# Optimization experiments

Measured on AMD Instinct MI355X. Metric: run time of the kernel, lower is better.

## Reference

```python
import jax, jax.numpy as jnp
import numpy as np

B, H, W, DIM = 8, 32, 32, 768
HEADS = 12
HD = DIM // HEADS  # 64


def setup_inputs() -> dict:
    key = jax.random.key(0)
    ks = jax.random.split(key, 7)
    s = 0.02  # init scale to keep logits in a sane range
    return {
        "x": jax.random.normal(ks[0], (B, H, W, DIM), jnp.float32),
        "qkv_w": jax.random.normal(ks[1], (3 * DIM, DIM), jnp.float32) * s,
        "qkv_b": jax.random.normal(ks[2], (3 * DIM,), jnp.float32) * s,
        "proj_w": jax.random.normal(ks[3], (DIM, DIM), jnp.float32) * s,
        "proj_b": jax.random.normal(ks[4], (DIM,), jnp.float32) * s,
        "rel_pos_h": jax.random.normal(ks[5], (2 * H - 1, HD), jnp.float32) * s,
        "rel_pos_w": jax.random.normal(ks[6], (2 * W - 1, HD), jnp.float32) * s,
    }


def reference(x, qkv_w, qkv_b, proj_w, proj_b, rel_pos_h, rel_pos_w):
    b, h, w, dim = x.shape
    n = h * w
    hd = dim // HEADS
    scale = hd ** -0.5

    xf = x.reshape(b, n, dim)
    qkv = xf @ qkv_w.T + qkv_b                       # (B, N, 3*dim)
    qkv = qkv.reshape(b, n, 3, HEADS, hd)
    qkv = jnp.transpose(qkv, (2, 0, 3, 1, 4)).reshape(3, b * HEADS, n, hd)
    q, k, v = qkv[0], qkv[1], qkv[2]                 # each (B*heads, N, hd)

    # decomposed rel-pos bias (q_size == k_size -> pure index lookup)
    coords_h = jnp.arange(h)[:, None] - jnp.arange(h)[None, :] + (h - 1)
    coords_w = jnp.arange(w)[:, None] - jnp.arange(w)[None, :] + (w - 1)
    Rh = rel_pos_h[coords_h]                         # (H, H, hd)
    Rw = rel_pos_w[coords_w]                         # (W, W, hd)
    r_q = q.reshape(b * HEADS, h, w, hd)
    rel_h = jnp.einsum('bhwc,hkc->bhwk', r_q, Rh)    # (B*heads, H, W, H)
    rel_w = jnp.einsum('bhwc,wkc->bhwk', r_q, Rw)    # (B*heads, H, W, W)
    bias = (rel_h[:, :, :, :, None] + rel_w[:, :, :, None, :]).reshape(b * HEADS, n, n)

    attn = (q * scale) @ jnp.swapaxes(k, -2, -1) + bias
    attn = jax.nn.softmax(attn, axis=-1)
    out = attn @ v                                   # (B*heads, N, hd)

    out = out.reshape(b, HEADS, n, hd)
    out = jnp.transpose(out, (0, 2, 1, 3)).reshape(b, n, dim)
    out = out @ proj_w.T + proj_b
    return out.reshape(b, h, w, dim)
```

## Files before the change

### kernel.cpp

```cpp
#include <hip/hip_runtime.h>
#include <hip/hip_bf16.h>

typedef unsigned short u16;
typedef __attribute__((ext_vector_type(8))) short bf16x8;
typedef __attribute__((ext_vector_type(4))) short s16x4;
typedef __attribute__((ext_vector_type(4))) float f32x4;

#define QSCALE 0.18033688011116012f
#define RPSCALE 8.0f
#define EXP2(x) __builtin_amdgcn_exp2f(x)

__device__ __forceinline__ float bf2f(u16 u) {
  union { unsigned int i; float f; } v; v.i = ((unsigned int)u) << 16; return v.f;
}
__device__ __forceinline__ u16 f2bf(float f) {
  union { float f; unsigned int i; } v; v.f = f;
  unsigned int r = v.i + 0x7fffu + ((v.i >> 16) & 1u);
  return (u16)(r >> 16);
}
__device__ __forceinline__ unsigned int pk2bf(float a, float b) {
  union { __hip_bfloat162 h; unsigned int u; } cv;
  cv.h = __float22bfloat162_rn(float2{a, b});
  return cv.u;
}
__device__ __forceinline__ f32x4 MFMA(bf16x8 a, bf16x8 b, f32x4 c) {
  return __builtin_amdgcn_mfma_f32_16x16x32_bf16(a, b, c, 0, 0, 0);
}
__device__ __forceinline__ void cvt8(const float* p, uint4* dst) {
  float4 f0 = *(const float4*)(p);
  float4 f1 = *(const float4*)(p + 4);
  u16* t = (u16*)dst;
  t[0] = f2bf(f0.x); t[1] = f2bf(f0.y); t[2] = f2bf(f0.z); t[3] = f2bf(f0.w);
  t[4] = f2bf(f1.x); t[5] = f2bf(f1.y); t[6] = f2bf(f1.z); t[7] = f2bf(f1.w);
}
__device__ __forceinline__ void cvt8s(const float* p, uint4* dst, float s) {
  float4 f0 = *(const float4*)(p);
  float4 f1 = *(const float4*)(p + 4);
  u16* t = (u16*)dst;
  t[0] = f2bf(f0.x * s); t[1] = f2bf(f0.y * s); t[2] = f2bf(f0.z * s); t[3] = f2bf(f0.w * s);
  t[4] = f2bf(f1.x * s); t[5] = f2bf(f1.y * s); t[6] = f2bf(f1.z * s); t[7] = f2bf(f1.w * s);
}
__device__ __forceinline__ void gld16(const u16* g, u16* l) {
  __builtin_amdgcn_global_load_lds(
      (const __attribute__((address_space(1))) unsigned int*)g,
      (__attribute__((address_space(3))) unsigned int*)l, 16, 0, 0);
}

#define N8_X  786432
#define N8_QW 221184
#define N8_PW 73728
__global__ __launch_bounds__(256) void cast_kernel(
    const float* __restrict__ x, const float* __restrict__ qw, const float* __restrict__ pw,
    u16* __restrict__ xb, u16* __restrict__ qwb, u16* __restrict__ pwb)
{
  const int i = blockIdx.x * 256 + threadIdx.x;
  const float* s; u16* d; int off;
  if (i < N8_X)            { s = x;  d = xb;  off = i; }
  else if (i < N8_X+N8_QW) { s = qw; d = qwb; off = i - N8_X; }
  else                     { s = pw; d = pwb; off = i - (N8_X + N8_QW); }
  uint4 pk; cvt8(s + (size_t)off * 8, &pk);
  *(uint4*)(d + (size_t)off * 8) = pk;
}

template<int MODE, int NXB>
__global__ __launch_bounds__(256) void gemm_bt(
    const u16* __restrict__ A, const u16* __restrict__ Bw, const float* __restrict__ bias,
    void* __restrict__ C0v, u16* __restrict__ C1, u16* __restrict__ C2,
    int M, int N, int K)
{
  __shared__ u16 sA[128 * 32];
  __shared__ u16 sB[128 * 32];
  const int tid = threadIdx.x;
  const int lane = tid & 63, wv = tid >> 6;
  const int wr = wv >> 1, wc = wv & 1;
  const int l16 = lane & 15, quad = lane >> 4;
  const int bi = blockIdx.x;
  const int t = bi >> 3;
  const int nx = t % NXB;
  const int my = ((t / NXB) << 3) | (bi & 7);
  const int m0 = my << 7, n0 = nx << 7;

  const int srow = tid >> 2, scol = (tid & 3) << 3;
  const u16* gA0 = A  + (size_t)(m0 + srow) * K + scol;
  const u16* gB0 = Bw + (size_t)(n0 + srow) * K + scol;
  const u16* gA1 = gA0 + (size_t)64 * K;
  const u16* gB1 = gB0 + (size_t)64 * K;
  u16* const lwA0 = sA + wv * 512;
  u16* const lwA1 = sA + 2048 + wv * 512;
  u16* const lwB0 = sB + wv * 512;
  u16* const lwB1 = sB + 2048 + wv * 512;

  f32x4 acc[4][4];
  #pragma unroll
  for (int i = 0; i < 4; ++i)
    #pragma unroll
    for (int j = 0; j < 4; ++j) {
      acc[i][j][0] = 0.f; acc[i][j][1] = 0.f; acc[i][j][2] = 0.f; acc[i][j][3] = 0.f;
    }

  for (int k0 = 0; k0 < K; k0 += 32) {
    __syncthreads();
    gld16(gA0 + k0, lwA0);
    gld16(gA1 + k0, lwA1);
    gld16(gB0 + k0, lwB0);
    gld16(gB1 + k0, lwB1);
    __syncthreads();
    bf16x8 af[4], bfr[4];
    #pragma unroll
    for (int i = 0; i < 4; ++i)
      af[i] = *(const bf16x8*)(sA + (wr * 64 + i * 16 + l16) * 32 + quad * 8);
    #pragma unroll
    for (int j = 0; j < 4; ++j)
      bfr[j] = *(const bf16x8*)(sB + (wc * 64 + j * 16 + l16) * 32 + quad * 8);
    #pragma unroll
    for (int i = 0; i < 4; ++i)
      #pragma unroll
      for (int j = 0; j < 4; ++j)
        acc[i][j] = MFMA(af[i], bfr[j], acc[i][j]);
  }

  #pragma unroll
  for (int j = 0; j < 4; ++j) {
    const int n = n0 + wc * 64 + j * 16 + l16;
    const float bv = bias[n];
    if (MODE == 0) {
      float* C0 = (float*)C0v;
      #pragma unroll
      for (int i = 0; i < 4; ++i) {
        const int m = m0 + wr * 64 + i * 16 + quad * 4;
        #pragma unroll
        for (int r = 0; r < 4; ++r)
          C0[(size_t)(m + r) * N + n] = acc[i][j][r] + bv;
      }
    } else {
      u16* C0 = (u16*)C0v;
      const int which = n / 768;
      const int rem = n - which * 768;
      const int head = rem >> 6, c = rem & 63;
      #pragma unroll
      for (int i = 0; i < 4; ++i) {
        const int m = m0 + wr * 64 + i * 16 + quad * 4;
        const int b = m >> 10, npos = m & 1023;
        const size_t bh = (size_t)(b * 12 + head);
        if (which == 0) {
          #pragma unroll
          for (int r = 0; r < 4; ++r)
            C0[(bh << 16) + ((size_t)(npos + r) << 6) + c] =
                f2bf((acc[i][j][r] + bv) * QSCALE);
        } else if (which == 1) {
          const size_t base = ((bh * 16 + (size_t)(npos >> 6)) << 12)
                            + (size_t)((((npos >> 4) & 3) * 2 + (c >> 5)) << 9)
                            + (size_t)((((npos & 15) + 16 * ((c >> 3) & 3)) << 3) + (c & 7));
          #pragma unroll
          for (int r = 0; r < 4; ++r)
            C1[base + r * 8] = f2bf(acc[i][j][r] + bv);
        } else {
          const size_t base = ((bh * 16 + (size_t)(npos >> 6)) << 12)
                            + (size_t)(((((npos >> 5) & 1) * 4 + (c >> 4))) << 9)
                            + (size_t)((((c & 15) + 16 * ((npos >> 3) & 3)) << 3) + (npos & 7));
          s16x4 pk;
          #pragma unroll
          for (int r = 0; r < 4; ++r) pk[r] = (short)f2bf(acc[i][j][r] + bv);
          *(s16x4*)(C2 + base) = pk;
        }
      }
    }
  }
}

__global__ __launch_bounds__(256) void attn_kernel(
    const u16* __restrict__ Q, const u16* __restrict__ Kf, const u16* __restrict__ Vf,
    const float* __restrict__ rph, const float* __restrict__ rpw,
    u16* __restrict__ Oa)
{
  __shared__ __align__(16) u16 uni[9216];
  __shared__ u16 sSh[4 * 32 * 36];

  u16* const uRPH = uni;
  u16* const uRPW = uni + 4536;

  const int tid = threadIdx.x;
  const int wave = tid >> 6, lane = tid & 63;
  const int l16 = lane & 15, quad = lane >> 4;
  const int bi = blockIdx.x;
  const int t = bi >> 3;
  const int qb = t & 7;
  const int bh = ((t >> 3) << 3) | (bi & 7);
  const int qrow0 = (qb << 7) + (wave << 5);
  const int qh = qrow0 >> 5;

  u16* const pw = uni + wave * 2304;
  u16* const sShw = sSh + wave * 1152;

  bf16x8 qf[2][2];
  #pragma unroll
  for (int qt = 0; qt < 2; ++qt) {
    const u16* qp = Q + (((size_t)bh << 10) + qrow0 + qt * 16 + l16) * 64 + quad * 8;
    qf[qt][0] = *(const bf16x8*)(qp);
    qf[qt][1] = *(const bf16x8*)(qp + 32);
  }

  for (int j = tid; j < 64 * 8; j += 256) {
    const int row = j >> 3, ck = (j & 7) << 3;
    uint4 vw;
    if (row < 63) cvt8s(rpw + (size_t)row * 64 + ck, &vw, RPSCALE);
    else { vw.x = 0u; vw.y = 0u; vw.z = 0u; vw.w = 0u; }
    *(uint4*)(uRPW + row * 72 + ck) = vw;
    if (row < 63) {
      uint4 vh;
      cvt8s(rph + (size_t)row * 64 + ck, &vh, RPSCALE);
      *(uint4*)(uRPH + row * 72 + ck) = vh;
    }
  }
  __syncthreads();

  #pragma unroll
  for (int qt = 0; qt < 2; ++qt)
    #pragma unroll
    for (int tk = 0; tk < 2; ++tk) {
      const int kh = tk * 16 + l16;
      const u16* bp = uRPH + (qh + 31 - kh) * 72 + quad * 8;
      bf16x8 b0 = *(const bf16x8*)(bp);
      bf16x8 b1 = *(const bf16x8*)(bp + 32);
      f32x4 c; c[0] = 0.f; c[1] = 0.f; c[2] = 0.f; c[3] = 0.f;
      c = MFMA(qf[qt][0], b0, c);
      c = MFMA(qf[qt][1], b1, c);
      #pragma unroll
      for (int r = 0; r < 4; ++r)
        sShw[(qt * 16 + quad * 4 + r) * 36 + tk * 16 + l16] = f2bf(c[r]);
    }

  f32x4 swc[2][4];
  #pragma unroll
  for (int qt = 0; qt < 2; ++qt)
    #pragma unroll
    for (int tj = 0; tj < 4; ++tj) {
      const u16* bp = uRPW + (tj * 16 + l16) * 72 + quad * 8;
      bf16x8 b0 = *(const bf16x8*)(bp);
      bf16x8 b1 = *(const bf16x8*)(bp + 32);
      f32x4 c; c[0] = 0.f; c[1] = 0.f; c[2] = 0.f; c[3] = 0.f;
      c = MFMA(qf[qt][0], b0, c);
      c = MFMA(qf[qt][1], b1, c);
      swc[qt][tj] = c;
    }
  __syncthreads();

  #pragma unroll
  for (int qt = 0; qt < 2; ++qt)
    #pragma unroll
    for (int tj = 0; tj < 4; ++tj)
      #pragma unroll
      for (int r = 0; r < 4; ++r)
        pw[(qt * 16 + quad * 4 + r) * 72 + tj * 16 + l16] = f2bf(swc[qt][tj][r]);

  float rw[2][2][4];
  #pragma unroll
  for (int qt = 0; qt < 2; ++qt)
    #pragma unroll
    for (int hi = 0; hi < 2; ++hi)
      #pragma unroll
      for (int r = 0; r < 4; ++r) {
        const int kw = hi * 16 + quad * 4 + r;
        rw[qt][hi][r] = bf2f(pw[(qt * 16 + l16) * 72 + (qt * 16 + l16 - kw + 31)]);
      }

  f32x4 oacc[2][4];
  #pragma unroll
  for (int qt = 0; qt < 2; ++qt)
    #pragma unroll
    for (int nd = 0; nd < 4; ++nd) {
      oacc[qt][nd][0] = 0.f; oacc[qt][nd][1] = 0.f;
      oacc[qt][nd][2] = 0.f; oacc[qt][nd][3] = 0.f;
    }
  float lsum[2] = {0.f, 0.f};

  const u16* const Kfb = Kf + (((size_t)bh) << 16) + lane * 8;
  const u16* const Vfb = Vf + (((size_t)bh) << 16) + lane * 8;

  for (int kt = 0; kt < 16; ++kt) {
    const u16* Kp = Kfb + ((size_t)kt << 12);
    const u16* Vp = Vfb + ((size_t)kt << 12);
    bf16x8 kfr[8];
    #pragma unroll
    for (int m = 0; m < 8; ++m)
      kfr[m] = *(const bf16x8*)(Kp + (m << 9));
    #pragma unroll
    for (int m = 0; m < 8; ++m)
      asm volatile("" :: "v"(kfr[m]));

    float rh[2][2];
    #pragma unroll
    for (int qt = 0; qt < 2; ++qt) {
      const unsigned int w2 =
          *(const unsigned int*)(sShw + (qt * 16 + l16) * 36 + (kt << 1));
      rh[qt][0] = bf2f((u16)(w2 & 0xffffu));
      rh[qt][1] = bf2f((u16)(w2 >> 16));
    }

    #pragma unroll
    for (int qt = 0; qt < 2; ++qt) {
      f32x4 sacc[4];
      #pragma unroll
      for (int mk = 0; mk < 4; ++mk) {
        f32x4 t4; t4[0] = 0.f; t4[1] = 0.f; t4[2] = 0.f; t4[3] = 0.f;
        t4 = MFMA(kfr[mk * 2 + 0], qf[qt][0], t4);
        t4 = MFMA(kfr[mk * 2 + 1], qf[qt][1], t4);
        sacc[mk] = t4;
      }
      #pragma unroll
      for (int mk = 0; mk < 4; ++mk) {
        const float rhv = rh[qt][mk >> 1];
        const float* rwp = rw[qt][mk & 1];
        float e0 = EXP2(sacc[mk][0] + rhv + rwp[0]);
        float e1 = EXP2(sacc[mk][1] + rhv + rwp[1]);
        float e2 = EXP2(sacc[mk][2] + rhv + rwp[2]);
        float e3 = EXP2(sacc[mk][3] + rhv + rwp[3]);
        lsum[qt] += (e0 + e1) + (e2 + e3);
        uint2 pk2; pk2.x = pk2bf(e0, e1); pk2.y = pk2bf(e2, e3);
        *(uint2*)(pw + (qt * 16 + l16) * 72 + mk * 16 + quad * 4) = pk2;
      }
    }

    #pragma unroll
    for (int ks = 0; ks < 2; ++ks) {
      bf16x8 bv[4];
      #pragma unroll
      for (int nd = 0; nd < 4; ++nd)
        bv[nd] = *(const bf16x8*)(Vp + ((ks * 4 + nd) << 9));
      #pragma unroll
      for (int qt = 0; qt < 2; ++qt) {
        bf16x8 ap = *(const bf16x8*)(pw + (qt * 16 + l16) * 72 + ks * 32 + quad * 8);
        #pragma unroll
        for (int nd = 0; nd < 4; ++nd)
          oacc[qt][nd] = MFMA(bv[nd], ap, oacc[qt][nd]);
      }
    }
  }

  const int b = bh / 12, head = bh - b * 12;
  #pragma unroll
  for (int qt = 0; qt < 2; ++qt) {
    float ls = lsum[qt];
    ls += __shfl_xor(ls, 16);
    ls += __shfl_xor(ls, 32);
    const float linv = 1.0f / ls;
    const size_t base =
        ((size_t)(b << 10) + qrow0 + qt * 16 + l16) * 768 + head * 64 + quad * 4;
    #pragma unroll
    for (int nd = 0; nd < 4; ++nd) {
      s16x4 pk;
      #pragma unroll
      for (int r = 0; r < 4; ++r) pk[r] = (short)f2bf(oacc[qt][nd][r] * linv);
      *(s16x4*)(Oa + base + nd * 16) = pk;
    }
  }
}

extern "C" void kernel_launch(void* const* d_in, const int* in_sizes, int n_in,
                              void* d_out, int out_size, void* d_ws, size_t ws_size,
                              hipStream_t stream) {
  (void)in_sizes; (void)n_in; (void)out_size; (void)ws_size;
  const float* x      = (const float*)d_in[0];
  const float* qkv_w  = (const float*)d_in[1];
  const float* qkv_b  = (const float*)d_in[2];
  const float* proj_w = (const float*)d_in[3];
  const float* proj_b = (const float*)d_in[4];
  const float* rph    = (const float*)d_in[5];
  const float* rpw    = (const float*)d_in[6];
  float* out = (float*)d_out;

  char* ws = (char*)d_ws;
  const size_t SZ = (size_t)96 * 1024 * 64;
  u16* Qw  = (u16*)ws;
  u16* Kfw = Qw + SZ;
  u16* Vfw = Kfw + SZ;
  u16* Xb  = Vfw + SZ;
  u16* Oa  = Xb;
  u16* QWb = Xb + SZ;
  u16* PWb = QWb + (size_t)2304 * 768;

  cast_kernel<<<4224, 256, 0, stream>>>(x, qkv_w, proj_w, Xb, QWb, PWb);
  gemm_bt<1, 18><<<1152, 256, 0, stream>>>(Xb, QWb, qkv_b, Qw, Kfw, Vfw, 8192, 2304, 768);
  attn_kernel<<<768, 256, 0, stream>>>(Qw, Kfw, Vfw, rph, rpw, Oa);
  gemm_bt<0, 6><<<384, 256, 0, stream>>>(Oa, PWb, proj_b, out, nullptr, nullptr, 8192, 768, 768);
}
```

Measured before the change: 211.8 us.

## Replace QKV GEMM with 256x256-tile 8-wave kernel using double-buffered LDS

Adds a dedicated QKV projection kernel that uses 256x256 output tiles, 512 threads (8 waves) and 128 KB of dynamic LDS. It double-buffers K-slices of 64, with direct global-to-LDS loads interleaved between four MFMA phases per step. The larger tiles raise operand reuse and cut global traffic, and the fused epilogue writes Q, K and V in the layouts the attention kernel expects. In exchange the grid shrinks to 288 blocks, which risks tail imbalance on 256 CUs, and the kernel carries higher register and LDS pressure.

```diff
diff --git a/kernel.cpp b/kernel.cpp
--- a/kernel.cpp
+++ b/kernel.cpp
@@ -60,6 +60,143 @@
   else                     { s = pw; d = pwb; off = i - (N8_X + N8_QW); }
   uint4 pk; cvt8(s + (size_t)off * 8, &pk);
   *(uint4*)(d + (size_t)off * 8) = pk;
+}
+
+__global__ __launch_bounds__(512) void gemm_qkv_8p(
+    const u16* __restrict__ A, const u16* __restrict__ Bw, const float* __restrict__ bias,
+    u16* __restrict__ Cq, u16* __restrict__ C1, u16* __restrict__ C2)
+{
+  extern __shared__ u16 lds[];
+  u16* const sA = lds;
+  u16* const sB = lds + 32768;
+  const int tid = threadIdx.x;
+  const int w = tid >> 6, lane = tid & 63;
+  const int l16 = lane & 15, quad = lane >> 4;
+  const int bi = blockIdx.x;
+  const int u = bi >> 3;
+  const int tm = ((u & 3) << 3) | (bi & 7);
+  const int tn = u >> 2;
+  const int m0 = tm << 8, n0 = tn << 8;
+
+  const int srow = (w << 3) + (lane >> 3);
+  const int sslot = (((lane & 7) ^ (lane >> 3)) << 3);
+  const int wch = w << 9;
+  const int s7 = l16 & 7;
+  const int sl0 = ((quad ^ s7) << 3);
+  const int sl1 = (((4 + quad) ^ s7) << 3);
+
+#define STAGE_A8(cb, kt, h) do { \
+    const u16* g_ = A + (size_t)(m0 + (h)*128 + srow)*768 + (kt)*64 + sslot; \
+    gld16(g_,              sA + (cb)*16384 + (h)*8192 + wch); \
+    gld16(g_ + 64*768,     sA + (cb)*16384 + (h)*8192 + 4096 + wch); \
+  } while (0)
+#define STAGE_B8(cb, kt, h) do { \
+    const u16* g_ = Bw + (size_t)(n0 + (h)*128 + srow)*768 + (kt)*64 + sslot; \
+    gld16(g_,              sB + (cb)*16384 + (h)*8192 + wch); \
+    gld16(g_ + 64*768,     sB + (cb)*16384 + (h)*8192 + 4096 + wch); \
+  } while (0)
+
+  f32x4 acc[16][2];
+  #pragma unroll
+  for (int i = 0; i < 16; ++i)
+    #pragma unroll
+    for (int j = 0; j < 2; ++j) {
+      acc[i][j][0] = 0.f; acc[i][j][1] = 0.f; acc[i][j][2] = 0.f; acc[i][j][3] = 0.f;
+    }
+
+  STAGE_B8(0, 0, 0);
+  STAGE_B8(0, 0, 1);
+  STAGE_A8(0, 0, 0);
+  STAGE_A8(0, 0, 1);
+  asm volatile("s_waitcnt vmcnt(2)" ::: "memory");
+  __builtin_amdgcn_s_barrier();
+
+#define PHASE8(mq, STAGE_STMT, TAIL_STMT) { \
+    bf16x8 af[4][2]; \
+    _Pragma("unroll") \
+    for (int i = 0; i < 4; ++i) { \
+      const u16* ap_ = aRd + ((mq)*64 + i*16)*64; \
+      af[i][0] = *(const bf16x8*)(ap_ + sl0); \
+      af[i][1] = *(const bf16x8*)(ap_ + sl1); \
+    } \
+    STAGE_STMT; \
+    __builtin_amdgcn_s_barrier(); \
+    asm volatile("s_waitcnt lgkmcnt(0)" ::: "memory"); \
+    __builtin_amdgcn_sched_barrier(0); \
+    __builtin_amdgcn_s_setprio(1); \
+    _Pragma("unroll") \
+    for (int i = 0; i < 4; ++i) { \
+      acc[(mq)*4+i][0] = MFMA(af[i][0], bq[0][0], acc[(mq)*4+i][0]); \
+      acc[(mq)*4+i][0] = MFMA(af[i][1], bq[0][1], acc[(mq)*4+i][0]); \
+      acc[(mq)*4+i][1] = MFMA(af[i][0], bq[1][0], acc[(mq)*4+i][1]); \
+      acc[(mq)*4+i][1] = MFMA(af[i][1], bq[1][1], acc[(mq)*4+i][1]); \
+    } \
+    __builtin_amdgcn_s_setprio(0); \
+    TAIL_STMT; \
+    __builtin_amdgcn_s_barrier(); \
+  }
+
+  int cur = 0;
+  #pragma unroll 1
+  for (int t = 0; t < 12; ++t) {
+    const int t1 = (t < 11) ? t + 1 : 11;
+    const int nb = cur ^ 1;
+    const u16* aRd = sA + cur * 16384 + l16 * 64;
+    bf16x8 bq[2][2];
+    {
+      const u16* bp = sB + cur * 16384 + (w * 32 + l16) * 64;
+      bq[0][0] = *(const bf16x8*)(bp + sl0);
+      bq[0][1] = *(const bf16x8*)(bp + sl1);
+      bq[1][0] = *(const bf16x8*)(bp + 1024 + sl0);
+      bq[1][1] = *(const bf16x8*)(bp + 1024 + sl1);
+    }
+    PHASE8(0, STAGE_B8(nb, t1, 0), {});
+    PHASE8(1, STAGE_B8(nb, t1, 1), asm volatile("s_waitcnt vmcnt(4)" ::: "memory"));
+    PHASE8(2, STAGE_A8(nb, t1, 0), {});
+    PHASE8(3, STAGE_A8(nb, t1, 1), asm volatile("s_waitcnt vmcnt(2)" ::: "memory"));
+    cur = nb;
+  }
+#undef PHASE8
+#undef STAGE_A8
+#undef STAGE_B8
+
+  asm volatile("s_waitcnt vmcnt(0)" ::: "memory");
+
+  const int which = tn / 3;
+  #pragma unroll
+  for (int j = 0; j < 2; ++j) {
+    const int n = n0 + w * 32 + j * 16 + l16;
+    const float bv = bias[n];
+    const int rem = n - which * 768;
+    const int head = rem >> 6, c = rem & 63;
+    #pragma unroll
+    for (int i = 0; i < 16; ++i) {
+      const int m = m0 + i * 16 + quad * 4;
+      const int b = m >> 10, npos = m & 1023;
+      const size_t bh = (size_t)(b * 12 + head);
+      if (which == 0) {
+        #pragma unroll
+        for (int r = 0; r < 4; ++r)
+          Cq[(bh << 16) + ((size_t)(npos + r) << 6) + c] =
+              f2bf((acc[i][j][r] + bv) * QSCALE);
+      } else if (which == 1) {
+        const size_t base = ((bh * 16 + (size_t)(npos >> 6)) << 12)
+                          + (size_t)((((npos >> 4) & 3) * 2 + (c >> 5)) << 9)
+                          + (size_t)((((npos & 15) + 16 * ((c >> 3) & 3)) << 3) + (c & 7));
+        #pragma unroll
+        for (int r = 0; r < 4; ++r)
+          C1[base + r * 8] = f2bf(acc[i][j][r] + bv);
+      } else {
+        const size_t base = ((bh * 16 + (size_t)(npos >> 6)) << 12)
+                          + (size_t)(((((npos >> 5) & 1) * 4 + (c >> 4))) << 9)
+                          + (size_t)((((c & 15) + 16 * ((npos >> 3) & 3)) << 3) + (npos & 7));
+        s16x4 pk;
+        #pragma unroll
+        for (int r = 0; r < 4; ++r) pk[r] = (short)f2bf(acc[i][j][r] + bv);
+        *(s16x4*)(C2 + base) = pk;
+      }
+    }
+  }
 }
 
 template<int MODE, int NXB>
@@ -379,8 +516,15 @@
   u16* QWb = Xb + SZ;
   u16* PWb = QWb + (size_t)2304 * 768;
 
+  static bool attr_set = false;
+  if (!attr_set) {
+    (void)hipFuncSetAttribute((const void*)gemm_qkv_8p,
+                              hipFuncAttributeMaxDynamicSharedMemorySize, 131072);
+    attr_set = true;
+  }
+
   cast_kernel<<<4224, 256, 0, stream>>>(x, qkv_w, proj_w, Xb, QWb, PWb);
-  gemm_bt<1, 18><<<1152, 256, 0, stream>>>(Xb, QWb, qkv_b, Qw, Kfw, Vfw, 8192, 2304, 768);
+  gemm_qkv_8p<<<288, 512, 131072, stream>>>(Xb, QWb, qkv_b, Qw, Kfw, Vfw);
   attn_kernel<<<768, 256, 0, stream>>>(Qw, Kfw, Vfw, rph, rpw, Oa);
   gemm_bt<0, 6><<<384, 256, 0, stream>>>(Oa, PWb, proj_b, out, nullptr, nullptr, 8192, 768, 768);
 }
```

Measured after the change: 213.4 us. No clear change (+0.8%).

## Triple-buffer GEMM shared-memory tiles with async prefetch two steps ahead

Applied to the files above, without the earlier changes.

Replaces the single-buffered load/sync/compute GEMM loop with a three-stage LDS ring. The next-next K tile is issued via direct global-to-LDS loads while MFMAs consume the current tile, synchronised with vmcnt waits and a single barrier per step. This aims to hide global memory latency behind compute in the QKV and projection GEMMs, at the cost of three times the LDS use per block and possibly lower occupancy.

```diff
diff --git a/kernel.cpp b/kernel.cpp
--- a/kernel.cpp
+++ b/kernel.cpp
@@ -68,16 +68,16 @@
     void* __restrict__ C0v, u16* __restrict__ C1, u16* __restrict__ C2,
     int M, int N, int K)
 {
-  __shared__ u16 sA[128 * 32];
-  __shared__ u16 sB[128 * 32];
+  __shared__ u16 sA[3][128 * 32];
+  __shared__ u16 sB[3][128 * 32];
   const int tid = threadIdx.x;
   const int lane = tid & 63, wv = tid >> 6;
   const int wr = wv >> 1, wc = wv & 1;
   const int l16 = lane & 15, quad = lane >> 4;
   const int bi = blockIdx.x;
-  const int t = bi >> 3;
-  const int nx = t % NXB;
-  const int my = ((t / NXB) << 3) | (bi & 7);
+  const int t0_ = bi >> 3;
+  const int nx = t0_ % NXB;
+  const int my = ((t0_ / NXB) << 3) | (bi & 7);
   const int m0 = my << 7, n0 = nx << 7;
 
   const int srow = tid >> 2, scol = (tid & 3) << 3;
@@ -85,10 +85,13 @@
   const u16* gB0 = Bw + (size_t)(n0 + srow) * K + scol;
   const u16* gA1 = gA0 + (size_t)64 * K;
   const u16* gB1 = gB0 + (size_t)64 * K;
-  u16* const lwA0 = sA + wv * 512;
-  u16* const lwA1 = sA + 2048 + wv * 512;
-  u16* const lwB0 = sB + wv * 512;
-  u16* const lwB1 = sB + 2048 + wv * 512;
+
+#define STAGE(b, k0) do { \
+    gld16(gA0 + (k0), sA[b] + wv * 512); \
+    gld16(gA1 + (k0), sA[b] + 2048 + wv * 512); \
+    gld16(gB0 + (k0), sB[b] + wv * 512); \
+    gld16(gB1 + (k0), sB[b] + 2048 + wv * 512); \
+  } while (0)
 
   f32x4 acc[4][4];
   #pragma unroll
@@ -98,26 +101,61 @@
       acc[i][j][0] = 0.f; acc[i][j][1] = 0.f; acc[i][j][2] = 0.f; acc[i][j][3] = 0.f;
     }
 
-  for (int k0 = 0; k0 < K; k0 += 32) {
-    __syncthreads();
-    gld16(gA0 + k0, lwA0);
-    gld16(gA1 + k0, lwA1);
-    gld16(gB0 + k0, lwB0);
-    gld16(gB1 + k0, lwB1);
-    __syncthreads();
-    bf16x8 af[4], bfr[4];
-    #pragma unroll
-    for (int i = 0; i < 4; ++i)
-      af[i] = *(const bf16x8*)(sA + (wr * 64 + i * 16 + l16) * 32 + quad * 8);
-    #pragma unroll
-    for (int j = 0; j < 4; ++j)
-      bfr[j] = *(const bf16x8*)(sB + (wc * 64 + j * 16 + l16) * 32 + quad * 8);
-    #pragma unroll
-    for (int i = 0; i < 4; ++i)
-      #pragma unroll
-      for (int j = 0; j < 4; ++j)
-        acc[i][j] = MFMA(af[i], bfr[j], acc[i][j]);
-  }
+  const int NT = K >> 5;
+  STAGE(0, 0);
+  STAGE(1, 32);
+
+#define STEP_BODY(cb) \
+    __builtin_amdgcn_s_barrier(); \
+    __builtin_amdgcn_sched_barrier(0); \
+    { \
+      bf16x8 af[4], bfr[4]; \
+      _Pragma("unroll") \
+      for (int i = 0; i < 4; ++i) \
+        af[i] = *(const bf16x8*)(sA[cb] + (wr * 64 + i * 16 + l16) * 32 + quad * 8); \
+      _Pragma("unroll") \
+      for (int j = 0; j < 4; ++j) \
+        bfr[j] = *(const bf16x8*)(sB[cb] + (wc * 64 + j * 16 + l16) * 32 + quad * 8); \
+      _Pragma("unroll") \
+      for (int i = 0; i < 4; ++i) \
+        _Pragma("unroll") \
+        for (int j = 0; j < 4; ++j) \
+          acc[i][j] = MFMA(af[i], bfr[j], acc[i][j]); \
+    }
+
+  int cb = 0;
+  #pragma unroll 1
+  for (int t = 0; t < NT - 1; ++t) {
+    asm volatile("s_waitcnt vmcnt(4)" ::: "memory");
+    if (t + 2 < NT) {
+      const int nbuf = (cb + 2 >= 3) ? cb - 1 : cb + 2;
+      const int k2 = (t + 2) << 5;
+      __builtin_amdgcn_s_barrier();
+      __builtin_amdgcn_sched_barrier(0);
+      STAGE(nbuf, k2);
+      {
+        bf16x8 af[4], bfr[4];
+        #pragma unroll
+        for (int i = 0; i < 4; ++i)
+          af[i] = *(const bf16x8*)(sA[cb] + (wr * 64 + i * 16 + l16) * 32 + quad * 8);
+        #pragma unroll
+        for (int j = 0; j < 4; ++j)
+          bfr[j] = *(const bf16x8*)(sB[cb] + (wc * 64 + j * 16 + l16) * 32 + quad * 8);
+        #pragma unroll
+        for (int i = 0; i < 4; ++i)
+          #pragma unroll
+          for (int j = 0; j < 4; ++j)
+            acc[i][j] = MFMA(af[i], bfr[j], acc[i][j]);
+      }
+    } else {
+      STEP_BODY(cb)
+    }
+    cb = (cb + 1 >= 3) ? 0 : cb + 1;
+  }
+  asm volatile("s_waitcnt vmcnt(0)" ::: "memory");
+  STEP_BODY(cb)
+#undef STEP_BODY
+#undef STAGE
 
   #pragma unroll
   for (int j = 0; j < 4; ++j) {
```

Result: slower. 238.2 us (+12.5%).

## Double GEMM K-step to 64 with XOR-swizzled LDS and retile proj GEMM

Applied to the files above, without the earlier changes.

The bf16 GEMM now stages 64-wide K slices per iteration instead of 32, halving the number of barrier pairs. It XOR-swizzles the LDS layout so the wider row reads avoid bank conflicts. The kernel is templated on the N tile width, and the output projection uses a 128x96 tile with 512 blocks instead of 128x128 with 384, to fill more CUs. LDS use per block doubles, which may lower occupancy, and the staging is still single-buffered.

```diff
diff --git a/kernel.cpp b/kernel.cpp
--- a/kernel.cpp
+++ b/kernel.cpp
@@ -62,66 +62,77 @@
   *(uint4*)(d + (size_t)off * 8) = pk;
 }
 
-template<int MODE, int NXB>
+template<int MODE, int NXB, int NJ>
 __global__ __launch_bounds__(256) void gemm_bt(
     const u16* __restrict__ A, const u16* __restrict__ Bw, const float* __restrict__ bias,
     void* __restrict__ C0v, u16* __restrict__ C1, u16* __restrict__ C2,
     int M, int N, int K)
 {
-  __shared__ u16 sA[128 * 32];
-  __shared__ u16 sB[128 * 32];
+  __shared__ u16 sA[128 * 64];
+  __shared__ u16 sB[NJ * 32 * 64];
   const int tid = threadIdx.x;
   const int lane = tid & 63, wv = tid >> 6;
   const int wr = wv >> 1, wc = wv & 1;
   const int l16 = lane & 15, quad = lane >> 4;
   const int bi = blockIdx.x;
-  const int t = bi >> 3;
-  const int nx = t % NXB;
-  const int my = ((t / NXB) << 3) | (bi & 7);
-  const int m0 = my << 7, n0 = nx << 7;
-
-  const int srow = tid >> 2, scol = (tid & 3) << 3;
-  const u16* gA0 = A  + (size_t)(m0 + srow) * K + scol;
-  const u16* gB0 = Bw + (size_t)(n0 + srow) * K + scol;
-  const u16* gA1 = gA0 + (size_t)64 * K;
-  const u16* gB1 = gB0 + (size_t)64 * K;
-  u16* const lwA0 = sA + wv * 512;
-  u16* const lwA1 = sA + 2048 + wv * 512;
-  u16* const lwB0 = sB + wv * 512;
-  u16* const lwB1 = sB + 2048 + wv * 512;
-
-  f32x4 acc[4][4];
+  const int t0_ = bi >> 3;
+  const int nx = t0_ % NXB;
+  const int my = ((t0_ / NXB) << 3) | (bi & 7);
+  const int m0 = my << 7, n0 = nx * (NJ * 32);
+
+  const int rs = tid >> 3;
+  const int gsl = (((tid & 7) ^ (rs & 7)) << 3);
+  const int wch = wv << 9;
+  const u16* gA0 = A  + (size_t)(m0 + rs) * K + gsl;
+  const u16* gB0 = Bw + (size_t)(n0 + rs) * K + gsl;
+
+#define STAGE(k0) do { \
+    _Pragma("unroll") \
+    for (int r_ = 0; r_ < 4; ++r_) \
+      gld16(gA0 + (size_t)r_ * 32 * K + (k0), sA + r_ * 2048 + wch); \
+    _Pragma("unroll") \
+    for (int r_ = 0; r_ < NJ; ++r_) \
+      gld16(gB0 + (size_t)r_ * 32 * K + (k0), sB + r_ * 2048 + wch); \
+  } while (0)
+
+  const int s7 = l16 & 7;
+  const int sl[2] = { ((quad ^ s7) << 3), (((4 + quad) ^ s7) << 3) };
+
+  f32x4 acc[4][NJ];
   #pragma unroll
   for (int i = 0; i < 4; ++i)
     #pragma unroll
-    for (int j = 0; j < 4; ++j) {
+    for (int j = 0; j < NJ; ++j) {
       acc[i][j][0] = 0.f; acc[i][j][1] = 0.f; acc[i][j][2] = 0.f; acc[i][j][3] = 0.f;
     }
 
-  for (int k0 = 0; k0 < K; k0 += 32) {
+  const int NT = K >> 6;
+  #pragma unroll 1
+  for (int t = 0; t < NT; ++t) {
     __syncthreads();
-    gld16(gA0 + k0, lwA0);
-    gld16(gA1 + k0, lwA1);
-    gld16(gB0 + k0, lwB0);
-    gld16(gB1 + k0, lwB1);
+    STAGE(t << 6);
     __syncthreads();
-    bf16x8 af[4], bfr[4];
-    #pragma unroll
-    for (int i = 0; i < 4; ++i)
-      af[i] = *(const bf16x8*)(sA + (wr * 64 + i * 16 + l16) * 32 + quad * 8);
-    #pragma unroll
-    for (int j = 0; j < 4; ++j)
-      bfr[j] = *(const bf16x8*)(sB + (wc * 64 + j * 16 + l16) * 32 + quad * 8);
-    #pragma unroll
-    for (int i = 0; i < 4; ++i)
-      #pragma unroll
-      for (int j = 0; j < 4; ++j)
-        acc[i][j] = MFMA(af[i], bfr[j], acc[i][j]);
-  }
-
-  #pragma unroll
-  for (int j = 0; j < 4; ++j) {
-    const int n = n0 + wc * 64 + j * 16 + l16;
+    #pragma unroll
+    for (int h = 0; h < 2; ++h) {
+      bf16x8 af[4], bfr[NJ];
+      #pragma unroll
+      for (int i = 0; i < 4; ++i)
+        af[i] = *(const bf16x8*)(sA + (wr * 64 + i * 16 + l16) * 64 + sl[h]);
+      #pragma unroll
+      for (int j = 0; j < NJ; ++j)
+        bfr[j] = *(const bf16x8*)(sB + (wc * (NJ * 16) + j * 16 + l16) * 64 + sl[h]);
+      #pragma unroll
+      for (int i = 0; i < 4; ++i)
+        #pragma unroll
+        for (int j = 0; j < NJ; ++j)
+          acc[i][j] = MFMA(af[i], bfr[j], acc[i][j]);
+    }
+  }
+#undef STAGE
+
+  #pragma unroll
+  for (int j = 0; j < NJ; ++j) {
+    const int n = n0 + wc * (NJ * 16) + j * 16 + l16;
     const float bv = bias[n];
     if (MODE == 0) {
       float* C0 = (float*)C0v;
@@ -380,7 +391,7 @@
   u16* PWb = QWb + (size_t)2304 * 768;
 
   cast_kernel<<<4224, 256, 0, stream>>>(x, qkv_w, proj_w, Xb, QWb, PWb);
-  gemm_bt<1, 18><<<1152, 256, 0, stream>>>(Xb, QWb, qkv_b, Qw, Kfw, Vfw, 8192, 2304, 768);
+  gemm_bt<1, 18, 4><<<1152, 256, 0, stream>>>(Xb, QWb, qkv_b, Qw, Kfw, Vfw, 8192, 2304, 768);
   attn_kernel<<<768, 256, 0, stream>>>(Qw, Kfw, Vfw, rph, rpw, Oa);
-  gemm_bt<0, 6><<<384, 256, 0, stream>>>(Oa, PWb, proj_b, out, nullptr, nullptr, 8192, 768, 768);
-}
+  gemm_bt<0, 8, 3><<<512, 256, 0, stream>>>(Oa, PWb, proj_b, out, nullptr, nullptr, 8192, 768, 768);
+}
```

Measured after the change: 209.7 us. About the same (-1.0%).
